# Kernel optimization log

Hardware: AMD Instinct MI355X
Metric: run time of the kernel (lower is better)

The kernel has to match this reference:

```python
import jax, jax.numpy as jnp
import numpy as np

N = 50000
H = 8          # heads
C = 10         # out channels per head
F_IN = 128
NEG_SLOPE = 0.2


def _glorot(key, shape, fan_in):
    return jax.random.normal(key, shape, dtype=jnp.float32) / np.sqrt(fan_in)


def setup_inputs() -> dict:
    key = jax.random.key(0)
    ks = jax.random.split(key, 16)
    x = jax.random.normal(ks[0], (N, F_IN), dtype=jnp.float32)
    edge_index = jax.random.randint(ks[1], (2, 1600000), 0, N, dtype=jnp.int64)
    inp = {"x": x, "edge_index": edge_index}
    dims = [F_IN, H * C, H * C]  # input dim of each of the 3 layers
    k = 2
    for i, din in enumerate(dims):
        inp[f"Wl{i}"] = _glorot(ks[k + 0], (din, H * C), din)
        inp[f"Wr{i}"] = _glorot(ks[k + 1], (din, H * C), din)
        inp[f"att{i}"] = _glorot(ks[k + 2], (H, C), C)
        inp[f"b{i}"] = jnp.zeros((H * C,), dtype=jnp.float32)
        k += 3
    return inp


def gatv2_layer(x, Wl, Wr, att, b, src, dst):
    # GATv2Conv (PyG defaults): separate lin_l/lin_r, e = att . leaky_relu(xl_j + xr_i),
    # segment softmax over incoming edges, scatter-add of alpha * xl_j, concat heads + bias.
    n = x.shape[0]
    xl = (x @ Wl).reshape(n, H, C)
    xr = (x @ Wr).reshape(n, H, C)
    e = jax.nn.leaky_relu(xl[src] + xr[dst], NEG_SLOPE)      # [E, H, C]
    score = jnp.einsum('ehc,hc->eh', e, att)                 # [E, H]
    smax = jax.ops.segment_max(score, dst, num_segments=n)   # [N, H]
    ex = jnp.exp(score - smax[dst])
    denom = jax.ops.segment_sum(ex, dst, num_segments=n)
    alpha = ex / (denom[dst] + 1e-16)                        # [E, H]
    out = jax.ops.segment_sum(alpha[:, :, None] * xl[src], dst, num_segments=n)
    return out.reshape(n, H * C) + b


def reference(x, edge_index, Wl0, Wr0, att0, b0, Wl1, Wr1, att1, b1, Wl2, Wr2, att2, b2):
    n = x.shape[0]
    # add_self_loops=True (PyG default)
    loop = jnp.arange(n, dtype=edge_index.dtype)
    src = jnp.concatenate([edge_index[0], loop])
    dst = jnp.concatenate([edge_index[1], loop])
    params = [(Wl0, Wr0, att0, b0), (Wl1, Wr1, att1, b1), (Wl2, Wr2, att2, b2)]
    for Wl, Wr, att, b in params:
        x = jax.nn.elu(gatv2_layer(x, Wl, Wr, att, b, src, dst))
    return x
```

## Files before the change

kernel.cpp:

```cpp
#include <hip/hip_runtime.h>
#include <hip/hip_bf16.h>
#include <hip/hip_fp16.h>

#define N_NODES 50000
#define HEADS 8
#define CHANS 10
#define HC 80
#define PADH 12
#define PHL 96
#define F_IN 128
#define E_EDGES 1600000
#define E_TOT (E_EDGES + N_NODES)
#define NEG_SLOPE 0.2f
#define NBUCK 3125
#define NCHUNK 128
#define CHUNK ((E_TOT + NCHUNK - 1) / NCHUNK)
#define XS_STRIDE 40
#define WS_STRIDE 40

typedef _Float16 f16x8 __attribute__((ext_vector_type(8)));
typedef float f32x4 __attribute__((ext_vector_type(4)));

#if __has_builtin(__builtin_amdgcn_fdot2) && __has_builtin(__builtin_elementwise_max)
#define USE_PK_SCORE 1
typedef _Float16 h2 __attribute__((ext_vector_type(2)));
#else
#define USE_PK_SCORE 0
#endif

__device__ inline void load_edge(const void* ei, int is64, int e, int& src, int& dst) {
    if (e < E_EDGES) {
        if (is64) {
            src = ((const int*)ei)[2 * e];
            dst = ((const int*)ei)[2 * (E_EDGES + e)];
        } else {
            src = ((const int*)ei)[e];
            dst = ((const int*)ei)[E_EDGES + e];
        }
    } else {
        src = dst = e - E_EDGES;
    }
}

__device__ inline int load_dst(const void* ei, int is64, int e) {
    if (e < E_EDGES) {
        if (is64) return ((const int*)ei)[2 * (E_EDGES + e)];
        return ((const int*)ei)[E_EDGES + e];
    }
    return e - E_EDGES;
}

__device__ inline int detect_is64(const void* ei, int tid, int* s_flag) {
    if (tid < 64) {
        const int* p = (const int*)ei;
        bool ok = (p[2 * tid + 1] == 0) && (p[2 * (tid + 64) + 1] == 0);
        unsigned long long m = __ballot(ok);
        if (tid == 0) *s_flag = (m == ~0ull) ? 1 : 0;
    }
    return 0;
}

__global__ __launch_bounds__(256) void hist_kernel(
        const void* ei, int* __restrict__ hist, int* __restrict__ bcount) {
    __shared__ int h[NBUCK];
    __shared__ int s_is64;
    int tid = threadIdx.x;
    for (int i = tid; i < NBUCK; i += 256) h[i] = 0;
    detect_is64(ei, tid, &s_is64);
    __syncthreads();
    int is64 = s_is64;
    int blk = blockIdx.x;
    int e0 = blk * CHUNK, e1 = min(e0 + CHUNK, E_TOT);
    for (int e = e0 + tid; e < e1; e += 4 * 256) {
        int d[4]; int cnt = 0;
        #pragma unroll
        for (int u = 0; u < 4; u++) {
            int ee = e + u * 256;
            if (ee < e1) { d[u] = load_dst(ei, is64, ee); cnt = u + 1; }
        }
        #pragma unroll
        for (int u = 0; u < 4; u++)
            if (u < cnt) atomicAdd(&h[d[u] >> 4], 1);
    }
    __syncthreads();
    for (int i = tid; i < NBUCK; i += 256) {
        int v = h[i];
        int old = v ? atomicAdd(&bcount[i], v) : 0;
        hist[blk * NBUCK + i] = old;
    }
}

__global__ void scan_total_kernel(const int* __restrict__ total, int* __restrict__ bbase) {
    __shared__ int wsum[16];
    __shared__ int wpre[16];
    __shared__ int carry;
    int tid = threadIdx.x;
    int lane = tid & 63, w = tid >> 6;
    if (tid == 0) carry = 0;
    __syncthreads();
    for (int base = 0; base < NBUCK; base += 1024) {
        int idx = base + tid;
        int v = (idx < NBUCK) ? total[idx] : 0;
        int sv = v;
        #pragma unroll
        for (int off = 1; off < 64; off <<= 1) {
            int t = __shfl_up(sv, off, 64);
            if (lane >= off) sv += t;
        }
        if (lane == 63) wsum[w] = sv;
        __syncthreads();
        if (w == 0) {
            int s = (lane < 16) ? wsum[lane] : 0;
            #pragma unroll
            for (int off = 1; off < 16; off <<= 1) {
                int t = __shfl_up(s, off, 64);
                if (lane >= off) s += t;
            }
            if (lane < 16) wpre[lane] = s;
        }
        __syncthreads();
        int pre = carry + ((w > 0) ? wpre[w - 1] : 0);
        if (idx < NBUCK) bbase[idx] = pre + sv - v;
        __syncthreads();
        if (tid == 0) carry += wpre[15];
        __syncthreads();
    }
}

__global__ __launch_bounds__(256) void scatter_sort_kernel(
        const void* ei, const int* __restrict__ hist, const int* __restrict__ bbase,
        int* __restrict__ tmp) {
    __shared__ int cur[NBUCK];
    __shared__ int s_is64;
    int tid = threadIdx.x;
    int blk = blockIdx.x;
    for (int i = tid; i < NBUCK; i += 256)
        cur[i] = bbase[i] + hist[blk * NBUCK + i];
    detect_is64(ei, tid, &s_is64);
    __syncthreads();
    int is64 = s_is64;
    int e0 = blk * CHUNK, e1 = min(e0 + CHUNK, E_TOT);
    for (int e = e0 + tid; e < e1; e += 4 * 256) {
        int s[4], d[4]; int cnt = 0;
        #pragma unroll
        for (int u = 0; u < 4; u++) {
            int ee = e + u * 256;
            if (ee < e1) { load_edge(ei, is64, ee, s[u], d[u]); cnt = u + 1; }
        }
        #pragma unroll
        for (int u = 0; u < 4; u++) {
            if (u < cnt) {
                int pos = atomicAdd(&cur[d[u] >> 4], 1);
                tmp[pos] = (s[u] << 4) | (d[u] & 15);
            }
        }
    }
}

__global__ __launch_bounds__(256) void node_sort_kernel(
        const int* __restrict__ tmp, const int* __restrict__ bbase,
        const int* __restrict__ total,
        int* __restrict__ adj, int* __restrict__ nstart, int* __restrict__ deg) {
    __shared__ int h16[16];
    __shared__ int st16[16];
    __shared__ int cur16[16];
    int tid = threadIdx.x;
    int b = blockIdx.x;
    int base = bbase[b];
    int n = total[b];
    if (tid < 16) h16[tid] = 0;
    __syncthreads();
    for (int k = tid; k < n; k += 256)
        atomicAdd(&h16[tmp[base + k] & 15], 1);
    __syncthreads();
    if (tid == 0) {
        int run = 0;
        #pragma unroll
        for (int c = 0; c < 16; c++) { st16[c] = run; cur16[c] = run; run += h16[c]; }
    }
    __syncthreads();
    for (int k = tid; k < n; k += 256) {
        int p = tmp[base + k];
        int pos = atomicAdd(&cur16[p & 15], 1);
        adj[base + pos] = p >> 4;
    }
    if (tid < 16) {
        nstart[b * 16 + tid] = base + st16[tid];
        deg[b * 16 + tid] = h16[tid];
    }
}

__global__ __launch_bounds__(256) void deghist_kernel(
        const int* __restrict__ deg, int* __restrict__ dh) {
    __shared__ int h[256];
    h[threadIdx.x] = 0;
    __syncthreads();
    int i = blockIdx.x * 256 + threadIdx.x;
    if (i < N_NODES) atomicAdd(&h[min(deg[i], 255)], 1);
    __syncthreads();
    if (h[threadIdx.x]) atomicAdd(&dh[threadIdx.x], h[threadIdx.x]);
}

__global__ void degscan_kernel(const int* __restrict__ dh, int* __restrict__ dcur) {
    __shared__ int s[256];
    int tid = threadIdx.x;
    int idx = 255 - tid;
    int own = dh[idx];
    s[tid] = own;
    __syncthreads();
    for (int off = 1; off < 256; off <<= 1) {
        int t = (tid >= off) ? s[tid - off] : 0;
        __syncthreads();
        s[tid] += t;
        __syncthreads();
    }
    dcur[idx] = s[tid] - own;
}

__global__ __launch_bounds__(256) void degscatter_kernel(
        const int* __restrict__ deg, int* __restrict__ dcur, int* __restrict__ perm) {
    __shared__ int h[256];
    __shared__ int res[256];
    __shared__ int lc[256];
    int tid = threadIdx.x;
    h[tid] = 0; lc[tid] = 0;
    __syncthreads();
    int i = blockIdx.x * 256 + tid;
    int d = (i < N_NODES) ? min(deg[i], 255) : -1;
    if (d >= 0) atomicAdd(&h[d], 1);
    __syncthreads();
    res[tid] = h[tid] ? atomicAdd(&dcur[tid], h[tid]) : 0;
    __syncthreads();
    if (d >= 0) {
        int off = atomicAdd(&lc[d], 1);
        perm[res[d] + off] = i;
    }
}

__global__ void wconv_kernel(const float* __restrict__ Wl, const float* __restrict__ Wr,
                             int din, int padded_in, __half* __restrict__ wt) {
    int c = blockIdx.x;
    int kp = threadIdx.x;
    const float* W = (c < 80) ? Wl : Wr;
    int cc = (c < 80) ? c : c - 80;
    float v = 0.f;
    if (padded_in) {
        int hh = kp / PADH, c2 = kp - hh * PADH;
        if (kp < PHL && c2 < CHANS)
            v = W[(hh * CHANS + c2) * 80 + cc];
    } else {
        if (kp < din) v = W[kp * 80 + cc];
    }
    wt[c * 128 + kp] = __float2half_rn(v);
}

__global__ __launch_bounds__(256) void gemm_mfma_kernel(
        const void* __restrict__ xin, int in_fp16, int nkt,
        const __half* __restrict__ wt,
        __half* __restrict__ xlh, float* __restrict__ xr) {
    __shared__ __half xs[64 * XS_STRIDE];
    __shared__ __half ws[160 * WS_STRIDE];
    int tid = threadIdx.x;
    int n0 = blockIdx.x * 64;
    int w = tid >> 6, lane = tid & 63;
    int quad = lane >> 4, r = lane & 15;

    f32x4 acc[10];
    #pragma unroll
    for (int t = 0; t < 10; t++) acc[t] = (f32x4){0.f, 0.f, 0.f, 0.f};

    int snode = tid >> 2;
    int sk = (tid & 3) * 8;
    int sg = n0 + snode;

    for (int kt = 0; kt < nkt; kt++) {
        f16x8 xv = (f16x8){0, 0, 0, 0, 0, 0, 0, 0};
        if (sg < N_NODES) {
            if (in_fp16) {
                uint4 u = *(const uint4*)((const __half*)xin + (size_t)sg * PHL + kt * 32 + sk);
                xv = __builtin_bit_cast(f16x8, u);
            } else {
                const float4* p = (const float4*)((const float*)xin + (size_t)sg * F_IN + kt * 32 + sk);
                float4 f0 = p[0], f1 = p[1];
                xv[0] = (_Float16)f0.x; xv[1] = (_Float16)f0.y;
                xv[2] = (_Float16)f0.z; xv[3] = (_Float16)f0.w;
                xv[4] = (_Float16)f1.x; xv[5] = (_Float16)f1.y;
                xv[6] = (_Float16)f1.z; xv[7] = (_Float16)f1.w;
            }
        }
        __syncthreads();
        *(uint4*)(&xs[snode * XS_STRIDE + sk]) = __builtin_bit_cast(uint4, xv);
        for (int u = tid; u < 640; u += 256) {
            int c = u >> 2, k8 = (u & 3) * 8;
            uint4 wv = *(const uint4*)(wt + c * 128 + kt * 32 + k8);
            *(uint4*)(&ws[c * WS_STRIDE + k8]) = wv;
        }
        __syncthreads();
        f16x8 a = __builtin_bit_cast(f16x8,
                     *(const uint4*)(&xs[(w * 16 + r) * XS_STRIDE + quad * 8]));
        #pragma unroll
        for (int ct = 0; ct < 10; ct++) {
            f16x8 bf = __builtin_bit_cast(f16x8,
                          *(const uint4*)(&ws[(ct * 16 + r) * WS_STRIDE + quad * 8]));
            acc[ct] = __builtin_amdgcn_mfma_f32_16x16x32_f16(a, bf, acc[ct], 0, 0, 0);
        }
    }
    #pragma unroll
    for (int ct = 0; ct < 10; ct++) {
        int col = ct * 16 + r;
        #pragma unroll
        for (int reg = 0; reg < 4; reg++) {
            int node = n0 + w * 16 + quad * 4 + reg;
            if (node < N_NODES) {
                float v = acc[ct][reg];
                if (col < 80) {
                    int hh = col / 10, cc = col - hh * 10;
                    xlh[(size_t)node * PHL + hh * PADH + cc] = __float2half_rn(v);
                } else {
                    xr[(size_t)node * HC + (col - 80)] = v;
                }
            }
        }
    }
}

__device__ inline void cvt10(uint2 a, uint2 b, uint2 c, float* v) {
    __half2 h;
    h = *(__half2*)&a.x; v[0] = __low2float(h); v[1] = __high2float(h);
    h = *(__half2*)&a.y; v[2] = __low2float(h); v[3] = __high2float(h);
    h = *(__half2*)&b.x; v[4] = __low2float(h); v[5] = __high2float(h);
    h = *(__half2*)&b.y; v[6] = __low2float(h); v[7] = __high2float(h);
    h = *(__half2*)&c.x; v[8] = __low2float(h); v[9] = __high2float(h);
}

__global__ __launch_bounds__(256, 4) void agg_kernel(
        const __half* __restrict__ xlh, const float* __restrict__ xr,
        const float* __restrict__ att, const float* __restrict__ bias,
        const int* __restrict__ nstart, const int* __restrict__ deg,
        const int* __restrict__ adj, const int* __restrict__ perm,
        __half* __restrict__ ybuf, float* __restrict__ yout) {
    int tid = threadIdx.x;
    int b = blockIdx.x;
    int h = tid & 7;
    int split = (tid >> 3) & 1;
    int i_local = tid >> 4;
    int node = perm[b * 16 + i_local];

    int s0 = nstart[node];
    int dg = deg[node];
    int cnt0 = (dg + 1) >> 1;
    int cnt = split ? (dg - cnt0) : cnt0;
    int k0 = s0 + split * cnt0;

#if USE_PK_SCORE
    h2 xrh[5], atth[5];
    #pragma unroll
    for (int p = 0; p < 5; p++) {
        xrh[p] = (h2){(_Float16)xr[(size_t)node * HC + h * CHANS + 2 * p],
                      (_Float16)xr[(size_t)node * HC + h * CHANS + 2 * p + 1]};
        atth[p] = (h2){(_Float16)att[h * CHANS + 2 * p],
                       (_Float16)att[h * CHANS + 2 * p + 1]};
    }
    const h2 k02 = {(_Float16)NEG_SLOPE, (_Float16)NEG_SLOPE};
    auto score_pk = [&](uint2 a, uint2 bq, uint2 cq) {
        unsigned int wv[5] = {a.x, a.y, bq.x, bq.y, cq.x};
        float s = 0.f;
        #pragma unroll
        for (int p = 0; p < 5; p++) {
            h2 v = __builtin_bit_cast(h2, wv[p]);
            h2 t = v + xrh[p];
            h2 tl = __builtin_elementwise_max(t, t * k02);
            s = __builtin_amdgcn_fdot2(tl, atth[p], s, false);
        }
        return s;
    };
#else
    float xr_c[CHANS], att_c[CHANS];
    #pragma unroll
    for (int c = 0; c < CHANS; c++) {
        xr_c[c]  = xr[(size_t)node * HC + h * CHANS + c];
        att_c[c] = att[h * CHANS + c];
    }
    auto score_pk = [&](uint2 a, uint2 bq, uint2 cq) {
        float v[CHANS];
        cvt10(a, bq, cq, v);
        float s = 0.f;
        #pragma unroll
        for (int c = 0; c < CHANS; c++) {
            float t = v[c] + xr_c[c];
            t = (t > 0.f) ? t : NEG_SLOPE * t;
            s += att_c[c] * t;
        }
        return s;
    };
#endif

    float m = -INFINITY, l = 0.f;
    float acc[CHANS];
    #pragma unroll
    for (int c = 0; c < CHANS; c++) acc[c] = 0.f;

    int kk = 0;
    for (; kk + 8 <= cnt; kk += 8) {
        uint2 ra[8], rb[8], rc[8];
        #pragma unroll
        for (int r = 0; r < 8; r++) {
            int j = adj[k0 + kk + r];
            const uint2* p = (const uint2*)(xlh + (size_t)j * PHL + h * PADH);
            ra[r] = p[0]; rb[r] = p[1]; rc[r] = p[2];
        }
        float sc[8];
        #pragma unroll
        for (int r = 0; r < 8; r++) sc[r] = score_pk(ra[r], rb[r], rc[r]);
        float mb = m;
        #pragma unroll
        for (int r = 0; r < 8; r++) mb = fmaxf(mb, sc[r]);
        float scale = __expf(m - mb);
        float ps = 0.f;
        #pragma unroll
        for (int r = 0; r < 8; r++) { sc[r] = __expf(sc[r] - mb); ps += sc[r]; }
        l = l * scale + ps;
        #pragma unroll
        for (int c = 0; c < CHANS; c++) acc[c] *= scale;
        #pragma unroll
        for (int r = 0; r < 8; r++) {
            float v[CHANS];
            cvt10(ra[r], rb[r], rc[r], v);
            #pragma unroll
            for (int c = 0; c < CHANS; c++) acc[c] += sc[r] * v[c];
        }
        m = mb;
    }
    for (; kk < cnt; kk++) {
        int j = adj[k0 + kk];
        const uint2* p = (const uint2*)(xlh + (size_t)j * PHL + h * PADH);
        uint2 a = p[0], bq = p[1], cq = p[2];
        float s = score_pk(a, bq, cq);
        float v[CHANS];
        cvt10(a, bq, cq, v);
        float mn = fmaxf(m, s);
        float scale = __expf(m - mn);
        float pp = __expf(s - mn);
        l = l * scale + pp;
        #pragma unroll
        for (int c = 0; c < CHANS; c++) acc[c] = acc[c] * scale + pp * v[c];
        m = mn;
    }

    float m2 = __shfl_xor(m, 8, 64);
    float l2 = __shfl_xor(l, 8, 64);
    float mn = fmaxf(m, m2);
    float sc1 = __expf(m - mn), sc2 = __expf(m2 - mn);
    float lt = l * sc1 + l2 * sc2;
    float accm[CHANS];
    #pragma unroll
    for (int c = 0; c < CHANS; c++) {
        float a2 = __shfl_xor(acc[c], 8, 64);
        accm[c] = acc[c] * sc1 + a2 * sc2;
    }
    if (split == 0) {
        float inv = 1.f / (lt + 1e-16f);
        float z[CHANS];
        #pragma unroll
        for (int c = 0; c < CHANS; c++) {
            float t = accm[c] * inv + bias[h * CHANS + c];
            z[c] = (t > 0.f) ? t : (__expf(t) - 1.f);
        }
        if (yout) {
            #pragma unroll
            for (int c = 0; c < CHANS; c++)
                yout[(size_t)node * HC + h * CHANS + c] = z[c];
        } else {
            __half2 h0 = __halves2half2(__float2half_rn(z[0]), __float2half_rn(z[1]));
            __half2 h1 = __halves2half2(__float2half_rn(z[2]), __float2half_rn(z[3]));
            __half2 h2v = __halves2half2(__float2half_rn(z[4]), __float2half_rn(z[5]));
            __half2 h3 = __halves2half2(__float2half_rn(z[6]), __float2half_rn(z[7]));
            __half2 h4 = __halves2half2(__float2half_rn(z[8]), __float2half_rn(z[9]));
            __half2 h5 = __halves2half2(__half(0.f), __half(0.f));
            uint2* dst = (uint2*)(ybuf + (size_t)node * PHL + h * PADH);
            dst[0] = make_uint2(*(unsigned*)&h0, *(unsigned*)&h1);
            dst[1] = make_uint2(*(unsigned*)&h2v, *(unsigned*)&h3);
            dst[2] = make_uint2(*(unsigned*)&h4, *(unsigned*)&h5);
        }
    }
}

extern "C" void kernel_launch(void* const* d_in, const int* in_sizes, int n_in,
                              void* d_out, int out_size, void* d_ws, size_t ws_size,
                              hipStream_t stream) {
    const float* x_in = (const float*)d_in[0];
    const void*  ei   = d_in[1];
    const float* Wl[3] = {(const float*)d_in[2], (const float*)d_in[6],  (const float*)d_in[10]};
    const float* Wr[3] = {(const float*)d_in[3], (const float*)d_in[7],  (const float*)d_in[11]};
    const float* At[3] = {(const float*)d_in[4], (const float*)d_in[8],  (const float*)d_in[12]};
    const float* Bi[3] = {(const float*)d_in[5], (const float*)d_in[9],  (const float*)d_in[13]};
    float* out = (float*)d_out;

    char* ws = (char*)d_ws;
    size_t off = 0;
    auto alloc = [&](size_t bytes) {
        void* p = ws + off;
        off += (bytes + 255) & ~(size_t)255;
        return p;
    };
    __half* xlh   = (__half*)alloc((size_t)N_NODES * PHL * sizeof(__half));
    float*  xr    = (float*)alloc((size_t)N_NODES * HC * sizeof(float));
    __half* buf16 = (__half*)alloc((size_t)N_NODES * PHL * sizeof(__half));
    __half* wt    = (__half*)alloc((size_t)3 * 160 * 128 * sizeof(__half));
    int*   tmp    = (int*)alloc((size_t)E_TOT * sizeof(int));
    int*   adj    = (int*)alloc((size_t)E_TOT * sizeof(int));
    int*   hist   = (int*)alloc((size_t)NCHUNK * NBUCK * sizeof(int));
    int*   bcount = (int*)alloc((size_t)NBUCK * sizeof(int));
    int*   bbase  = (int*)alloc((size_t)NBUCK * sizeof(int));
    int*   nstart = (int*)alloc((size_t)N_NODES * sizeof(int));
    int*   deg    = (int*)alloc((size_t)N_NODES * sizeof(int));
    int*   perm   = (int*)alloc((size_t)N_NODES * sizeof(int));
    int*   dh     = (int*)alloc(256 * sizeof(int));
    int*   dcur   = (int*)alloc(256 * sizeof(int));

    hipMemsetAsync(bcount, 0, (size_t)NBUCK * sizeof(int), stream);
    hipMemsetAsync(dh, 0, 256 * sizeof(int), stream);
    for (int layer = 0; layer < 3; layer++)
        wconv_kernel<<<160, 128, 0, stream>>>(Wl[layer], Wr[layer],
                                              layer == 0 ? F_IN : HC,
                                              layer == 0 ? 0 : 1,
                                              wt + (size_t)layer * 160 * 128);
    hist_kernel<<<NCHUNK, 256, 0, stream>>>(ei, hist, bcount);
    scan_total_kernel<<<1, 1024, 0, stream>>>(bcount, bbase);
    scatter_sort_kernel<<<NCHUNK, 256, 0, stream>>>(ei, hist, bbase, tmp);
    node_sort_kernel<<<NBUCK, 256, 0, stream>>>(tmp, bbase, bcount, adj, nstart, deg);
    int nblocks = (N_NODES + 255) / 256;
    deghist_kernel<<<nblocks, 256, 0, stream>>>(deg, dh);
    degscan_kernel<<<1, 256, 0, stream>>>(dh, dcur);
    degscatter_kernel<<<nblocks, 256, 0, stream>>>(deg, dcur, perm);

    int gemm_blocks = (N_NODES + 63) / 64;
    const void* cur = (const void*)x_in;
    int in_fp16 = 0;
    for (int layer = 0; layer < 3; layer++) {
        int nkt = (layer == 0) ? 4 : 3;
        gemm_mfma_kernel<<<gemm_blocks, 256, 0, stream>>>(
            cur, in_fp16, nkt, wt + (size_t)layer * 160 * 128, xlh, xr);
        __half* ybuf = (layer == 2) ? nullptr : buf16;
        float*  yout = (layer == 2) ? out : nullptr;
        agg_kernel<<<NBUCK, 256, 0, stream>>>(xlh, xr, At[layer], Bi[layer],
                                              nstart, deg, adj, perm, ybuf, yout);
        cur = (const void*)buf16;
        in_fp16 = 1;
    }
}
```

Before: 354.8 us.

## Split each node's edges four ways, enlarge GEMM tile, merge setup launches

The aggregation kernel now gives each node 32 threads (4 edge splits per head) instead of 16, and launches twice as many blocks. The partial softmax states are combined with a two-step butterfly shuffle. This aims at better load balance and more latency hiding on the gather-bound edge loop. The GEMM tile grows from 64 to 128 nodes per block so weight tiles are reused across two MFMA row tiles. The three weight-conversion launches become one, and the two memsets become one by placing the buffers next to each other. The extra splits add more shuffle and merge work per node and leave fewer edges per thread.

```diff
diff --git a/kernel.cpp b/kernel.cpp
--- a/kernel.cpp
+++ b/kernel.cpp
@@ -13,6 +13,7 @@
 #define E_TOT (E_EDGES + N_NODES)
 #define NEG_SLOPE 0.2f
 #define NBUCK 3125
+#define NAGG 6250
 #define NCHUNK 128
 #define CHUNK ((E_TOT + NCHUNK - 1) / NCHUNK)
 #define XS_STRIDE 40
@@ -237,87 +238,106 @@
     }
 }
 
-__global__ void wconv_kernel(const float* __restrict__ Wl, const float* __restrict__ Wr,
-                             int din, int padded_in, __half* __restrict__ wt) {
-    int c = blockIdx.x;
+__global__ void wconv_kernel(const float* __restrict__ Wl0, const float* __restrict__ Wr0,
+                             const float* __restrict__ Wl1, const float* __restrict__ Wr1,
+                             const float* __restrict__ Wl2, const float* __restrict__ Wr2,
+                             __half* __restrict__ wt) {
+    int g = blockIdx.x;
+    int layer = g / 160, c = g - layer * 160;
     int kp = threadIdx.x;
+    const float* Wl = (layer == 0) ? Wl0 : (layer == 1) ? Wl1 : Wl2;
+    const float* Wr = (layer == 0) ? Wr0 : (layer == 1) ? Wr1 : Wr2;
     const float* W = (c < 80) ? Wl : Wr;
     int cc = (c < 80) ? c : c - 80;
     float v = 0.f;
-    if (padded_in) {
+    if (layer == 0) {
+        if (kp < F_IN) v = W[kp * 80 + cc];
+    } else {
         int hh = kp / PADH, c2 = kp - hh * PADH;
         if (kp < PHL && c2 < CHANS)
             v = W[(hh * CHANS + c2) * 80 + cc];
-    } else {
-        if (kp < din) v = W[kp * 80 + cc];
-    }
-    wt[c * 128 + kp] = __float2half_rn(v);
+    }
+    wt[(size_t)g * 128 + kp] = __float2half_rn(v);
 }
 
 __global__ __launch_bounds__(256) void gemm_mfma_kernel(
         const void* __restrict__ xin, int in_fp16, int nkt,
         const __half* __restrict__ wt,
         __half* __restrict__ xlh, float* __restrict__ xr) {
-    __shared__ __half xs[64 * XS_STRIDE];
+    __shared__ __half xs[128 * XS_STRIDE];
     __shared__ __half ws[160 * WS_STRIDE];
     int tid = threadIdx.x;
-    int n0 = blockIdx.x * 64;
+    int n0 = blockIdx.x * 128;
     int w = tid >> 6, lane = tid & 63;
     int quad = lane >> 4, r = lane & 15;
 
-    f32x4 acc[10];
+    f32x4 acc[2][10];
     #pragma unroll
-    for (int t = 0; t < 10; t++) acc[t] = (f32x4){0.f, 0.f, 0.f, 0.f};
-
-    int snode = tid >> 2;
-    int sk = (tid & 3) * 8;
+    for (int nt = 0; nt < 2; nt++)
+        #pragma unroll
+        for (int t = 0; t < 10; t++) acc[nt][t] = (f32x4){0.f, 0.f, 0.f, 0.f};
+
+    int snode = tid >> 1;
+    int sk = (tid & 1) * 16;
     int sg = n0 + snode;
 
     for (int kt = 0; kt < nkt; kt++) {
-        f16x8 xv = (f16x8){0, 0, 0, 0, 0, 0, 0, 0};
+        f16x8 xv0 = (f16x8){0, 0, 0, 0, 0, 0, 0, 0}, xv1 = xv0;
         if (sg < N_NODES) {
             if (in_fp16) {
-                uint4 u = *(const uint4*)((const __half*)xin + (size_t)sg * PHL + kt * 32 + sk);
-                xv = __builtin_bit_cast(f16x8, u);
+                const uint4* p = (const uint4*)((const __half*)xin + (size_t)sg * PHL + kt * 32 + sk);
+                xv0 = __builtin_bit_cast(f16x8, p[0]);
+                xv1 = __builtin_bit_cast(f16x8, p[1]);
             } else {
                 const float4* p = (const float4*)((const float*)xin + (size_t)sg * F_IN + kt * 32 + sk);
-                float4 f0 = p[0], f1 = p[1];
-                xv[0] = (_Float16)f0.x; xv[1] = (_Float16)f0.y;
-                xv[2] = (_Float16)f0.z; xv[3] = (_Float16)f0.w;
-                xv[4] = (_Float16)f1.x; xv[5] = (_Float16)f1.y;
-                xv[6] = (_Float16)f1.z; xv[7] = (_Float16)f1.w;
+                float4 f0 = p[0], f1 = p[1], f2 = p[2], f3 = p[3];
+                xv0[0] = (_Float16)f0.x; xv0[1] = (_Float16)f0.y;
+                xv0[2] = (_Float16)f0.z; xv0[3] = (_Float16)f0.w;
+                xv0[4] = (_Float16)f1.x; xv0[5] = (_Float16)f1.y;
+                xv0[6] = (_Float16)f1.z; xv0[7] = (_Float16)f1.w;
+                xv1[0] = (_Float16)f2.x; xv1[1] = (_Float16)f2.y;
+                xv1[2] = (_Float16)f2.z; xv1[3] = (_Float16)f2.w;
+                xv1[4] = (_Float16)f3.x; xv1[5] = (_Float16)f3.y;
+                xv1[6] = (_Float16)f3.z; xv1[7] = (_Float16)f3.w;
             }
         }
         __syncthreads();
-        *(uint4*)(&xs[snode * XS_STRIDE + sk]) = __builtin_bit_cast(uint4, xv);
+        *(uint4*)(&xs[snode * XS_STRIDE + sk]) = __builtin_bit_cast(uint4, xv0);
+        *(uint4*)(&xs[snode * XS_STRIDE + sk + 8]) = __builtin_bit_cast(uint4, xv1);
         for (int u = tid; u < 640; u += 256) {
             int c = u >> 2, k8 = (u & 3) * 8;
             uint4 wv = *(const uint4*)(wt + c * 128 + kt * 32 + k8);
             *(uint4*)(&ws[c * WS_STRIDE + k8]) = wv;
         }
         __syncthreads();
-        f16x8 a = __builtin_bit_cast(f16x8,
-                     *(const uint4*)(&xs[(w * 16 + r) * XS_STRIDE + quad * 8]));
+        #pragma unroll
+        for (int nt = 0; nt < 2; nt++) {
+            f16x8 a = __builtin_bit_cast(f16x8,
+                         *(const uint4*)(&xs[(w * 32 + nt * 16 + r) * XS_STRIDE + quad * 8]));
+            #pragma unroll
+            for (int ct = 0; ct < 10; ct++) {
+                f16x8 bf = __builtin_bit_cast(f16x8,
+                              *(const uint4*)(&ws[(ct * 16 + r) * WS_STRIDE + quad * 8]));
+                acc[nt][ct] = __builtin_amdgcn_mfma_f32_16x16x32_f16(a, bf, acc[nt][ct], 0, 0, 0);
+            }
+        }
+    }
+    #pragma unroll
+    for (int nt = 0; nt < 2; nt++) {
         #pragma unroll
         for (int ct = 0; ct < 10; ct++) {
-            f16x8 bf = __builtin_bit_cast(f16x8,
-                          *(const uint4*)(&ws[(ct * 16 + r) * WS_STRIDE + quad * 8]));
-            acc[ct] = __builtin_amdgcn_mfma_f32_16x16x32_f16(a, bf, acc[ct], 0, 0, 0);
-        }
-    }
-    #pragma unroll
-    for (int ct = 0; ct < 10; ct++) {
-        int col = ct * 16 + r;
-        #pragma unroll
-        for (int reg = 0; reg < 4; reg++) {
-            int node = n0 + w * 16 + quad * 4 + reg;
-            if (node < N_NODES) {
-                float v = acc[ct][reg];
-                if (col < 80) {
-                    int hh = col / 10, cc = col - hh * 10;
-                    xlh[(size_t)node * PHL + hh * PADH + cc] = __float2half_rn(v);
-                } else {
-                    xr[(size_t)node * HC + (col - 80)] = v;
+            int col = ct * 16 + r;
+            #pragma unroll
+            for (int reg = 0; reg < 4; reg++) {
+                int node = n0 + w * 32 + nt * 16 + quad * 4 + reg;
+                if (node < N_NODES) {
+                    float v = acc[nt][ct][reg];
+                    if (col < 80) {
+                        int hh = col / 10, cc = col - hh * 10;
+                        xlh[(size_t)node * PHL + hh * PADH + cc] = __float2half_rn(v);
+                    } else {
+                        xr[(size_t)node * HC + (col - 80)] = v;
+                    }
                 }
             }
         }
@@ -342,15 +362,15 @@
     int tid = threadIdx.x;
     int b = blockIdx.x;
     int h = tid & 7;
-    int split = (tid >> 3) & 1;
-    int i_local = tid >> 4;
-    int node = perm[b * 16 + i_local];
+    int split = (tid >> 3) & 3;
+    int i_local = tid >> 5;
+    int node = perm[b * 8 + i_local];
 
     int s0 = nstart[node];
     int dg = deg[node];
-    int cnt0 = (dg + 1) >> 1;
-    int cnt = split ? (dg - cnt0) : cnt0;
-    int k0 = s0 + split * cnt0;
+    int base = dg >> 2, rem = dg & 3;
+    int cnt = base + (split < rem ? 1 : 0);
+    int k0 = s0 + split * base + min(split, rem);
 
 #if USE_PK_SCORE
     h2 xrh[5], atth[5];
@@ -395,7 +415,7 @@
     };
 #endif
 
-    float m = -INFINITY, l = 0.f;
+    float m = -1e30f, l = 0.f;
     float acc[CHANS];
     #pragma unroll
     for (int c = 0; c < CHANS; c++) acc[c] = 0.f;
@@ -447,23 +467,26 @@
         m = mn;
     }
 
-    float m2 = __shfl_xor(m, 8, 64);
-    float l2 = __shfl_xor(l, 8, 64);
-    float mn = fmaxf(m, m2);
-    float sc1 = __expf(m - mn), sc2 = __expf(m2 - mn);
-    float lt = l * sc1 + l2 * sc2;
-    float accm[CHANS];
     #pragma unroll
-    for (int c = 0; c < CHANS; c++) {
-        float a2 = __shfl_xor(acc[c], 8, 64);
-        accm[c] = acc[c] * sc1 + a2 * sc2;
+    for (int stride = 8; stride <= 16; stride <<= 1) {
+        float m2 = __shfl_xor(m, stride, 64);
+        float l2 = __shfl_xor(l, stride, 64);
+        float mn = fmaxf(m, m2);
+        float sc1 = __expf(m - mn), sc2 = __expf(m2 - mn);
+        l = l * sc1 + l2 * sc2;
+        #pragma unroll
+        for (int c = 0; c < CHANS; c++) {
+            float a2 = __shfl_xor(acc[c], stride, 64);
+            acc[c] = acc[c] * sc1 + a2 * sc2;
+        }
+        m = mn;
     }
     if (split == 0) {
-        float inv = 1.f / (lt + 1e-16f);
+        float inv = 1.f / (l + 1e-16f);
         float z[CHANS];
         #pragma unroll
         for (int c = 0; c < CHANS; c++) {
-            float t = accm[c] * inv + bias[h * CHANS + c];
+            float t = acc[c] * inv + bias[h * CHANS + c];
             z[c] = (t > 0.f) ? t : (__expf(t) - 1.f);
         }
         if (yout) {
@@ -511,20 +534,15 @@
     int*   adj    = (int*)alloc((size_t)E_TOT * sizeof(int));
     int*   hist   = (int*)alloc((size_t)NCHUNK * NBUCK * sizeof(int));
     int*   bcount = (int*)alloc((size_t)NBUCK * sizeof(int));
+    int*   dh     = (int*)alloc(256 * sizeof(int));
     int*   bbase  = (int*)alloc((size_t)NBUCK * sizeof(int));
     int*   nstart = (int*)alloc((size_t)N_NODES * sizeof(int));
     int*   deg    = (int*)alloc((size_t)N_NODES * sizeof(int));
     int*   perm   = (int*)alloc((size_t)N_NODES * sizeof(int));
-    int*   dh     = (int*)alloc(256 * sizeof(int));
     int*   dcur   = (int*)alloc(256 * sizeof(int));
 
-    hipMemsetAsync(bcount, 0, (size_t)NBUCK * sizeof(int), stream);
-    hipMemsetAsync(dh, 0, 256 * sizeof(int), stream);
-    for (int layer = 0; layer < 3; layer++)
-        wconv_kernel<<<160, 128, 0, stream>>>(Wl[layer], Wr[layer],
-                                              layer == 0 ? F_IN : HC,
-                                              layer == 0 ? 0 : 1,
-                                              wt + (size_t)layer * 160 * 128);
+    hipMemsetAsync(bcount, 0, (size_t)((char*)dh - (char*)bcount) + 1024, stream);
+    wconv_kernel<<<480, 128, 0, stream>>>(Wl[0], Wr[0], Wl[1], Wr[1], Wl[2], Wr[2], wt);
     hist_kernel<<<NCHUNK, 256, 0, stream>>>(ei, hist, bcount);
     scan_total_kernel<<<1, 1024, 0, stream>>>(bcount, bbase);
     scatter_sort_kernel<<<NCHUNK, 256, 0, stream>>>(ei, hist, bbase, tmp);
@@ -534,7 +552,7 @@
     degscan_kernel<<<1, 256, 0, stream>>>(dh, dcur);
     degscatter_kernel<<<nblocks, 256, 0, stream>>>(deg, dcur, perm);
 
-    int gemm_blocks = (N_NODES + 63) / 64;
+    int gemm_blocks = (N_NODES + 127) / 128;
     const void* cur = (const void*)x_in;
     int in_fp16 = 0;
     for (int layer = 0; layer < 3; layer++) {
@@ -543,8 +561,8 @@
             cur, in_fp16, nkt, wt + (size_t)layer * 160 * 128, xlh, xr);
         __half* ybuf = (layer == 2) ? nullptr : buf16;
         float*  yout = (layer == 2) ? out : nullptr;
-        agg_kernel<<<NBUCK, 256, 0, stream>>>(xlh, xr, At[layer], Bi[layer],
-                                              nstart, deg, adj, perm, ybuf, yout);
+        agg_kernel<<<NAGG, 256, 0, stream>>>(xlh, xr, At[layer], Bi[layer],
+                                             nstart, deg, adj, perm, ybuf, yout);
         cur = (const void*)buf16;
         in_fp16 = 1;
     }
```

Result: slower. 371.1 us (+4.6%).
